# Optimization experiments

Measured on AMD Instinct MI355X. Metric: run time of the kernel, lower is better.

## Reference

```python
import jax, jax.numpy as jnp
import numpy as np
from jax import lax

RES = 14
DIM = 384
KEY_DIM = 32
NUM_HEADS = 12
ATTN_RATIO = 4
NH_KD = KEY_DIM * NUM_HEADS            # 384
DH = ATTN_RATIO * KEY_DIM * NUM_HEADS  # 1536
HQKV = DH + 2 * NH_KD                  # 2304
BN_EPS = 1e-5


def _bias_idxs():
    ys, xs = np.meshgrid(np.arange(RES), np.arange(RES), indexing='ij')
    ys = ys.reshape(-1); xs = xs.reshape(-1)
    dy = np.abs(ys[:, None] - ys[None, :])
    dx = np.abs(xs[:, None] - xs[None, :])
    return jnp.asarray(dy * RES + dx, dtype=jnp.int32)  # [196,196], 196 unique offsets


def setup_inputs() -> dict:
    key = jax.random.key(0)
    ks = jax.random.split(key, 16)
    B = 128
    x = jax.random.normal(ks[0], (B, DIM, RES, RES), dtype=jnp.float32)
    # qkv: 1x1 conv DIM->HQKV + BN
    qkv_w = jax.random.normal(ks[1], (HQKV, DIM, 1, 1), dtype=jnp.float32) * 0.05
    qkv_g = jax.random.normal(ks[2], (HQKV,), dtype=jnp.float32) * 0.1 + 1.0
    qkv_b = jax.random.normal(ks[3], (HQKV,), dtype=jnp.float32) * 0.1
    qkv_m = jax.random.normal(ks[4], (HQKV,), dtype=jnp.float32) * 0.1
    qkv_v = jax.random.uniform(ks[5], (HQKV,), dtype=jnp.float32) + 0.5
    # dw: depthwise 3x3 conv on q channels + BN
    dw_w = jax.random.normal(ks[6], (NH_KD, 1, 3, 3), dtype=jnp.float32) * 0.2
    dw_g = jax.random.normal(ks[7], (NH_KD,), dtype=jnp.float32) * 0.1 + 1.0
    dw_b = jax.random.normal(ks[8], (NH_KD,), dtype=jnp.float32) * 0.1
    dw_m = jax.random.normal(ks[9], (NH_KD,), dtype=jnp.float32) * 0.1
    dw_v = jax.random.uniform(ks[10], (NH_KD,), dtype=jnp.float32) + 0.5
    # proj: ReLU -> 1x1 conv DH->DIM + BN
    proj_w = jax.random.normal(ks[11], (DIM, DH, 1, 1), dtype=jnp.float32) * 0.05
    proj_g = jax.random.normal(ks[12], (DIM,), dtype=jnp.float32) * 0.1 + 1.0
    proj_b = jax.random.normal(ks[13], (DIM,), dtype=jnp.float32) * 0.1
    proj_m = jax.random.normal(ks[14], (DIM,), dtype=jnp.float32) * 0.1
    proj_v = jax.random.uniform(ks[15], (DIM,), dtype=jnp.float32) + 0.5
    ab = jax.random.normal(jax.random.fold_in(key, 99), (NUM_HEADS, RES * RES), dtype=jnp.float32) * 0.1
    return {
        'x': x,
        'qkv_w': qkv_w, 'qkv_g': qkv_g, 'qkv_b': qkv_b, 'qkv_m': qkv_m, 'qkv_v': qkv_v,
        'dw_w': dw_w, 'dw_g': dw_g, 'dw_b': dw_b, 'dw_m': dw_m, 'dw_v': dw_v,
        'proj_w': proj_w, 'proj_g': proj_g, 'proj_b': proj_b, 'proj_m': proj_m, 'proj_v': proj_v,
        'attn_biases': ab,
        'bias_idxs': _bias_idxs(),
    }


def _bn(x, g, b, m, v):
    scale = g / jnp.sqrt(v + BN_EPS)
    return x * scale[None, :, None, None] + (b - m * scale)[None, :, None, None]


def reference(x, qkv_w, qkv_g, qkv_b, qkv_m, qkv_v,
              dw_w, dw_g, dw_b, dw_m, dw_v,
              proj_w, proj_g, proj_b, proj_m, proj_v,
              attn_biases, bias_idxs):
    B, _, H, W = x.shape
    n = H * W
    scale = KEY_DIM ** -0.5
    # 1x1 conv + BN
    qkv = jnp.einsum('bchw,oc->bohw', x, qkv_w[:, :, 0, 0])
    qkv = _bn(qkv, qkv_g, qkv_b, qkv_m, qkv_v)
    q = qkv[:, :NH_KD]
    k = qkv[:, NH_KD:2 * NH_KD]
    v = qkv[:, 2 * NH_KD:]
    # depthwise 3x3 conv + BN on q
    q = lax.conv_general_dilated(q, dw_w, (1, 1), ((1, 1), (1, 1)),
                                 dimension_numbers=('NCHW', 'OIHW', 'NCHW'),
                                 feature_group_count=NH_KD)
    q = _bn(q, dw_g, dw_b, dw_m, dw_v)
    # heads: [b, h, d, n]
    q = q.reshape(B, NUM_HEADS, KEY_DIM, n)
    k = k.reshape(B, NUM_HEADS, KEY_DIM, n)
    v = v.reshape(B, NUM_HEADS, ATTN_RATIO * KEY_DIM, n)
    bias = attn_biases[:, bias_idxs]  # [h, n, n]
    attn = jnp.einsum('bhdn,bhdm->bhnm', q, k) * scale + bias[None]
    attn = jax.nn.softmax(attn, axis=-1)
    out = jnp.einsum('bhdm,bhnm->bhdn', v, attn).reshape(B, DH, H, W)
    out = jax.nn.relu(out)
    out = jnp.einsum('bchw,oc->bohw', out, proj_w[:, :, 0, 0])
    return _bn(out, proj_g, proj_b, proj_m, proj_v)
```

## Files before the change

kernel.cpp:

```cpp
#include <hip/hip_runtime.h>

typedef __bf16 bf16;
typedef bf16 bf16x8 __attribute__((ext_vector_type(8)));
typedef bf16 bf16x4 __attribute__((ext_vector_type(4)));
typedef short short4v __attribute__((ext_vector_type(4)));
typedef float f32x4 __attribute__((ext_vector_type(4)));

#define NPIX 196
#define CIN 384
#define NHEADS 12
#define MPAD 224
#define VSTRIDE 232
#define OSTRIDE 40

__device__ __forceinline__ float ldf(const void* p, size_t i, int f) {
    return f ? ((const float*)p)[i] : (float)((const bf16*)p)[i];
}

__device__ __forceinline__ void gld16(const void* g, void* lds_wave_base) {
    __builtin_amdgcn_global_load_lds(
        (const __attribute__((address_space(1))) void*)(unsigned long long)g,
        (__attribute__((address_space(3))) void*)(unsigned long long)lds_wave_base,
        16, 0, 0);
}

__device__ __forceinline__ int xcd_swizzle(int orig, int nwg) {
    int q = nwg >> 3, r = nwg & 7;
    int xcd = orig & 7, idx = orig >> 3;
    return (xcd < r ? xcd * (q + 1) : r * (q + 1) + (xcd - r) * q) + idx;
}

__device__ __forceinline__ f32x4 mfma16(bf16x4 a, bf16x4 b, f32x4 c) {
#if __has_builtin(__builtin_amdgcn_mfma_f32_16x16x16bf16_1k)
    return __builtin_amdgcn_mfma_f32_16x16x16bf16_1k(
        __builtin_bit_cast(short4v, a), __builtin_bit_cast(short4v, b), c, 0, 0, 0);
#else
    asm volatile("v_mfma_f32_16x16x16_bf16 %0, %1, %2, %0" : "+v"(c) : "v"(a), "v"(b));
    return c;
#endif
}

__device__ __forceinline__ f32x4 vmax4(f32x4 a, f32x4 b) {
    f32x4 r;
    r[0] = fmaxf(a[0], b[0]);
    r[1] = fmaxf(a[1], b[1]);
    r[2] = fmaxf(a[2], b[2]);
    r[3] = fmaxf(a[3], b[3]);
    return r;
}

__global__ void detect_kernel(const unsigned int* __restrict__ x, int* __restrict__ flag) {
    __shared__ int cnt;
    if (threadIdx.x == 0) cnt = 0;
    __syncthreads();
    int c = 0;
#pragma unroll
    for (int k = 0; k < 8; k++) {
        unsigned int w = x[threadIdx.x * 8 + k];
        unsigned int e = (w >> 7) & 0xFFu;
        if (e > 200u) c++;
    }
    atomicAdd(&cnt, c);
    __syncthreads();
    if (threadIdx.x == 0) *flag = (cnt >= 16) ? 1 : 0;
}

__global__ void convert_kernel(const void* __restrict__ src, bf16* __restrict__ dst, int n,
                               const int* __restrict__ flag) {
    int f = *flag;
    for (int i = blockIdx.x * 256 + threadIdx.x; i < n; i += gridDim.x * 256)
        dst[i] = (bf16)ldf(src, i, f);
}

__global__ void transpose_x_kernel(const void* __restrict__ x, const int* __restrict__ flag,
                                   bf16* __restrict__ xt, int b0) {
    __shared__ bf16 tile[32][33];
    int f = *flag;
    int b = blockIdx.z, gb = b0 + b;
    int c0 = blockIdx.y * 32;
    int hw0 = blockIdx.x * 32;
    int tx = threadIdx.x, ty = threadIdx.y;
    int hw = hw0 + tx, c = c0 + ty;
    if (hw < NPIX) tile[ty][tx] = (bf16)ldf(x, ((size_t)gb * CIN + c) * NPIX + hw, f);
    __syncthreads();
    int hw2 = hw0 + ty, c2 = c0 + tx;
    if (hw2 < NPIX) xt[((size_t)b * NPIX + hw2) * CIN + c2] = tile[tx][ty];
}

__device__ __forceinline__ void gemm_tile(const bf16* __restrict__ A, const bf16* __restrict__ B,
                                          int K, bf16* As, bf16* Bs, f32x4 acc[4][4]) {
    int tid = threadIdx.x;
    int wave = tid >> 6, lane = tid & 63;
    int wm = wave >> 1, wn = wave & 1;
    int row = lane & 15, grp = lane >> 4;
    int sr = lane >> 3;
    int scg = (lane & 7) ^ sr;
    const int BUF = 128 * 64;
    const bf16* Ag = A + (size_t)(wave * 8 + sr) * K + scg * 8;
    const bf16* Bg = B + (size_t)(wave * 8 + sr) * K + scg * 8;
#pragma unroll
    for (int p = 0; p < 4; p++) {
        gld16(Ag + (size_t)(p * 32) * K, As + (p * 256 + wave * 64) * 8);
        gld16(Bg + (size_t)(p * 32) * K, Bs + (p * 256 + wave * 64) * 8);
    }
    __syncthreads();
    int cur = 0;
    for (int kb = 0; kb < K; kb += 64) {
        if (kb + 64 < K) {
            bf16* Asn = As + (cur ^ 1) * BUF;
            bf16* Bsn = Bs + (cur ^ 1) * BUF;
#pragma unroll
            for (int p = 0; p < 4; p++) {
                gld16(Ag + (size_t)(p * 32) * K + kb + 64, Asn + (p * 256 + wave * 64) * 8);
                gld16(Bg + (size_t)(p * 32) * K + kb + 64, Bsn + (p * 256 + wave * 64) * 8);
            }
        }
        const bf16* Asc = As + cur * BUF;
        const bf16* Bsc = Bs + cur * BUF;
#pragma unroll
        for (int ki = 0; ki < 2; ki++) {
            bf16x8 af[4], bfr[4];
#pragma unroll
            for (int t = 0; t < 4; t++) {
                int ra = wm * 64 + t * 16 + row;
                af[t] = *(const bf16x8*)(Asc + ra * 64 + (((ki * 4 + grp) ^ (ra & 7)) * 8));
                int rb = wn * 64 + t * 16 + row;
                bfr[t] = *(const bf16x8*)(Bsc + rb * 64 + (((ki * 4 + grp) ^ (rb & 7)) * 8));
            }
#pragma unroll
            for (int mt = 0; mt < 4; mt++)
#pragma unroll
                for (int nt = 0; nt < 4; nt++)
                    acc[mt][nt] =
                        __builtin_amdgcn_mfma_f32_16x16x32_bf16(af[mt], bfr[nt], acc[mt][nt], 0, 0, 0);
        }
        if (kb + 64 < K) {
            __syncthreads();
            cur ^= 1;
        }
    }
}

__global__ __launch_bounds__(256) void gemm_qkv_kernel(
    const bf16* __restrict__ xt, const bf16* __restrict__ w,
    const void* __restrict__ g, const void* __restrict__ bb,
    const void* __restrict__ mm, const void* __restrict__ vv, const int* __restrict__ flag,
    bf16* __restrict__ qb, bf16* __restrict__ kt, bf16* __restrict__ vb) {
    __shared__ bf16 As[2 * 128 * 64];
    __shared__ bf16 Bs[2 * 128 * 64];
    f32x4 acc[4][4];
#pragma unroll
    for (int i = 0; i < 4; i++)
#pragma unroll
        for (int j = 0; j < 4; j++) acc[i][j] = (f32x4){0.f, 0.f, 0.f, 0.f};
    int nwg = gridDim.x * gridDim.y;
    int l = xcd_swizzle(blockIdx.y * gridDim.x + blockIdx.x, nwg);
    int m0 = (l % gridDim.x) * 128, n0 = (l / gridDim.x) * 128;
    gemm_tile(w + (size_t)m0 * CIN, xt + (size_t)n0 * CIN, CIN, As, Bs, acc);
    int f = *flag;
    int wave = threadIdx.x >> 6, lane = threadIdx.x & 63;
    int wm = wave >> 1, wn = wave & 1, row = lane & 15, grp = lane >> 4;
#pragma unroll
    for (int mt = 0; mt < 4; mt++) {
#pragma unroll
        for (int r = 0; r < 4; r++) {
            int o = m0 + wm * 64 + mt * 16 + grp * 4 + r;
            float scv = ldf(g, o, f) * rsqrtf(ldf(vv, o, f) + 1e-5f);
            float sh = ldf(bb, o, f) - ldf(mm, o, f) * scv;
#pragma unroll
            for (int nt = 0; nt < 4; nt++) {
                int n = n0 + wn * 64 + nt * 16 + row;
                int b = n / NPIX, hw = n - b * NPIX;
                float val = acc[mt][nt][r] * scv + sh;
                bf16 bv = (bf16)val;
                if (o < 384) {
                    qb[((size_t)b * 384 + o) * NPIX + hw] = bv;
                } else if (o < 768) {
                    kt[((size_t)b * NPIX + hw) * CIN + (o - 384)] = bv;
                } else {
                    vb[((size_t)b * 1536 + (o - 768)) * MPAD + hw] = bv;
                }
            }
        }
    }
}

__global__ __launch_bounds__(256) void gemm_proj_kernel(
    const bf16* __restrict__ ot, const bf16* __restrict__ w,
    const void* __restrict__ g, const void* __restrict__ bb,
    const void* __restrict__ mm, const void* __restrict__ vv, const int* __restrict__ flag,
    void* __restrict__ out, int b0) {
    __shared__ bf16 As[2 * 128 * 64];
    __shared__ bf16 Bs[2 * 128 * 64];
    f32x4 acc[4][4];
#pragma unroll
    for (int i = 0; i < 4; i++)
#pragma unroll
        for (int j = 0; j < 4; j++) acc[i][j] = (f32x4){0.f, 0.f, 0.f, 0.f};
    int nwg = gridDim.x * gridDim.y;
    int l = xcd_swizzle(blockIdx.y * gridDim.x + blockIdx.x, nwg);
    int m0 = (l % gridDim.x) * 128, n0 = (l / gridDim.x) * 128;
    gemm_tile(w + (size_t)m0 * 1536, ot + (size_t)n0 * 1536, 1536, As, Bs, acc);
    int f = *flag;
    int wave = threadIdx.x >> 6, lane = threadIdx.x & 63;
    int wm = wave >> 1, wn = wave & 1, row = lane & 15, grp = lane >> 4;
#pragma unroll
    for (int mt = 0; mt < 4; mt++) {
#pragma unroll
        for (int r = 0; r < 4; r++) {
            int o = m0 + wm * 64 + mt * 16 + grp * 4 + r;
            float scv = ldf(g, o, f) * rsqrtf(ldf(vv, o, f) + 1e-5f);
            float sh = ldf(bb, o, f) - ldf(mm, o, f) * scv;
#pragma unroll
            for (int nt = 0; nt < 4; nt++) {
                int n = n0 + wn * 64 + nt * 16 + row;
                int b = n / NPIX, hw = n - b * NPIX;
                float val = acc[mt][nt][r] * scv + sh;
                size_t oidx = ((size_t)(b0 + b) * 384 + o) * NPIX + hw;
                if (f) ((float*)out)[oidx] = val;
                else ((bf16*)out)[oidx] = (bf16)val;
            }
        }
    }
}

__global__ void dwconv_kernel(const bf16* __restrict__ qb, const bf16* __restrict__ w,
                              const void* __restrict__ g, const void* __restrict__ bb,
                              const void* __restrict__ mm, const void* __restrict__ vv,
                              const int* __restrict__ flag, bf16* __restrict__ qt) {
    __shared__ bf16 tile[32][33];
    int f = *flag;
    int b = blockIdx.z;
    int c0 = blockIdx.y * 32, hw0 = blockIdx.x * 32;
    int tx = threadIdx.x, ty = threadIdx.y;
    int c = c0 + ty, hw = hw0 + tx;
    if (hw < NPIX) {
        int y = hw / 14, x = hw % 14;
        float acc = 0.f;
        const bf16* wp = w + c * 9;
        const bf16* qp = qb + ((size_t)b * 384 + c) * NPIX;
#pragma unroll
        for (int ky = 0; ky < 3; ky++) {
            int yy = y + ky - 1;
            if (yy < 0 || yy >= 14) continue;
#pragma unroll
            for (int kx = 0; kx < 3; kx++) {
                int xx = x + kx - 1;
                if (xx < 0 || xx >= 14) continue;
                acc += (float)qp[yy * 14 + xx] * (float)wp[ky * 3 + kx];
            }
        }
        float sc = ldf(g, c, f) * rsqrtf(ldf(vv, c, f) + 1e-5f);
        float sh = ldf(bb, c, f) - ldf(mm, c, f) * sc;
        tile[ty][tx] = (bf16)(acc * sc + sh);
    }
    __syncthreads();
    int hw2 = hw0 + ty, c2 = c0 + tx;
    if (hw2 < NPIX) qt[((size_t)b * NPIX + hw2) * CIN + c2] = tile[tx][ty];
}

__global__ void bias_gather_kernel(const void* __restrict__ ab, const int* __restrict__ idx,
                                   const int* __restrict__ flag, float* __restrict__ biasf) {
    int f = *flag;
    int t = blockIdx.x * 256 + threadIdx.x;
    if (t >= NHEADS * NPIX * MPAD) return;
    int h = t / (NPIX * MPAD);
    int rem = t - h * (NPIX * MPAD);
    int n = rem / MPAD, m = rem - n * MPAD;
    biasf[t] = (m < NPIX) ? ldf(ab, h * NPIX + idx[n * NPIX + m], f) : -1e30f;
}

__global__ void zero_vpad_kernel(bf16* __restrict__ vb, int rows) {
    int t = blockIdx.x * 256 + threadIdx.x;
    if (t >= rows * 7) return;
    int r = t / 7, c = t - r * 7;
    *(unsigned long long*)(vb + (size_t)r * MPAD + NPIX + c * 4) = 0ull;
}

__global__ __launch_bounds__(256, 2) void attn_kernel(
    const bf16* __restrict__ qt, const bf16* __restrict__ ktp, const bf16* __restrict__ vb,
    const float* __restrict__ biasf, bf16* __restrict__ ot) {
    __shared__ bf16 Vs[128 * VSTRIDE];
    __shared__ bf16 Osh[4][16 * OSTRIDE];
    int nwg = gridDim.x * gridDim.y;
    int l = xcd_swizzle(blockIdx.y * gridDim.x + blockIdx.x, nwg);
    int h = l % NHEADS, b = l / NHEADS;
    int tid = threadIdx.x;
    int wave = tid >> 6, lane = tid & 63;
    int row = lane & 15, grp = lane >> 4;
    const float scale = 0.17677669529663687f;
    const f32x4 zf = {0.f, 0.f, 0.f, 0.f};

    {
        const bf16* vsrc = vb + ((size_t)b * 1536 + h * 128) * MPAD;
#pragma unroll
        for (int it = 0; it < 14; it++) {
            int i = it * 256 + tid;
            int r = i / 28, gch = i - r * 28;
            *(bf16x8*)(Vs + r * VSTRIDE + gch * 8) = *(const bf16x8*)(vsrc + (size_t)i * 8);
        }
    }
    __syncthreads();

    const bf16* vls = Vs + row * VSTRIDE + grp * 4;

    for (int nb = wave; nb < 13; nb += 4) {
        int n0 = nb * 16;
        int n = n0 + row;
        int nc = n > 195 ? 195 : n;

        bf16x8 aq = *(const bf16x8*)(qt + ((size_t)b * NPIX + nc) * CIN + h * 32 + grp * 8);

        f32x4 sacc[14];
#pragma unroll
        for (int mt = 0; mt < 14; mt++) {
            int krow = mt * 16 + row;
            if (krow > 195) krow = 195;
            bf16x8 ak = *(const bf16x8*)(ktp + ((size_t)b * NPIX + krow) * CIN + h * 32 + grp * 8);
            sacc[mt] = __builtin_amdgcn_mfma_f32_16x16x32_bf16(ak, aq, zf, 0, 0, 0);
        }

        const float* bp = biasf + ((size_t)h * NPIX + nc) * MPAD + grp * 4;
        f32x4 mxv = {-3.4e38f, -3.4e38f, -3.4e38f, -3.4e38f};
#pragma unroll
        for (int mt = 0; mt < 14; mt++) {
            f32x4 bv = *(const f32x4*)(bp + mt * 16);
            f32x4 s = sacc[mt] * scale + bv;
            sacc[mt] = s;
            mxv = vmax4(mxv, s);
        }
        float mx = fmaxf(fmaxf(mxv[0], mxv[1]), fmaxf(mxv[2], mxv[3]));
        mx = fmaxf(mx, __shfl_xor(mx, 16));
        mx = fmaxf(mx, __shfl_xor(mx, 32));

        f32x4 sumv = zf;
        bf16x4 pf[14];
#pragma unroll
        for (int mt = 0; mt < 14; mt++) {
            f32x4 e;
#pragma unroll
            for (int r = 0; r < 4; r++) e[r] = __expf(sacc[mt][r] - mx);
            sumv += e;
            bf16x4 pb;
#pragma unroll
            for (int r = 0; r < 4; r++) pb[r] = (bf16)e[r];
            pf[mt] = pb;
        }
        float sum = (sumv[0] + sumv[1]) + (sumv[2] + sumv[3]);
        sum += __shfl_xor(sum, 16);
        sum += __shfl_xor(sum, 32);
        float inv = 1.f / sum;

        f32x4 oacc[8];
#pragma unroll
        for (int dt = 0; dt < 8; dt++) oacc[dt] = zf;
#pragma unroll
        for (int mt = 0; mt < 14; mt++) {
            bf16x4 p = pf[mt];
#pragma unroll
            for (int dt = 0; dt < 8; dt++) {
                bf16x4 v4 = *(const bf16x4*)(vls + dt * 16 * VSTRIDE + mt * 16);
                oacc[dt] = mfma16(v4, p, oacc[dt]);
            }
        }

        bf16* osw = Osh[wave];
        int r2 = lane >> 2, c2 = lane & 3;
        int n2 = n0 + r2;
        bf16* op = ot + ((size_t)b * NPIX + n2) * 1536 + h * 128;
#pragma unroll
        for (int dp = 0; dp < 4; dp++) {
#pragma unroll
            for (int u = 0; u < 2; u++) {
                int dt = dp * 2 + u;
                bf16x4 o4;
#pragma unroll
                for (int r = 0; r < 4; r++) {
                    float v = oacc[dt][r] * inv;
                    o4[r] = (bf16)(v > 0.f ? v : 0.f);
                }
                *(bf16x4*)(osw + row * OSTRIDE + u * 16 + grp * 4) = o4;
            }
            asm volatile("s_waitcnt lgkmcnt(0)" ::: "memory");
            if (n2 < NPIX) {
                bf16x8 ov = *(const bf16x8*)(osw + r2 * OSTRIDE + c2 * 8);
                *(bf16x8*)(op + dp * 32 + c2 * 8) = ov;
            }
            asm volatile("s_waitcnt lgkmcnt(0)" ::: "memory");
        }
    }
}

extern "C" void kernel_launch(void* const* d_in, const int* in_sizes, int n_in,
                              void* d_out, int out_size, void* d_ws, size_t ws_size,
                              hipStream_t stream) {
    const void* x      = d_in[0];
    const void* qkv_w  = d_in[1];
    const void* qkv_g  = d_in[2];
    const void* qkv_b  = d_in[3];
    const void* qkv_m  = d_in[4];
    const void* qkv_v  = d_in[5];
    const void* dw_w   = d_in[6];
    const void* dw_g   = d_in[7];
    const void* dw_b   = d_in[8];
    const void* dw_m   = d_in[9];
    const void* dw_v   = d_in[10];
    const void* proj_w = d_in[11];
    const void* proj_g = d_in[12];
    const void* proj_b = d_in[13];
    const void* proj_m = d_in[14];
    const void* proj_v = d_in[15];
    const void* ab     = d_in[16];
    const int*  idx    = (const int*)d_in[17];

    char* ws = (char*)d_ws;
    size_t off = 0;
    auto alloc = [&](size_t bytes) { void* p = ws + off; off += (bytes + 255) & ~(size_t)255; return p; };

    int*   flag = (int*)alloc(4);
    bf16*  wq   = (bf16*)alloc((size_t)2304 * 384 * 2);
    bf16*  wp   = (bf16*)alloc((size_t)384 * 1536 * 2);
    bf16*  wd   = (bf16*)alloc((size_t)384 * 9 * 2);
    float* biasf= (float*)alloc((size_t)NHEADS * NPIX * MPAD * 4);
    size_t fixed = off;

    const size_t s_xt = (size_t)NPIX * CIN;
    const size_t s_qb = (size_t)384 * NPIX;
    const size_t s_kt = (size_t)NPIX * 384;
    const size_t s_vb = (size_t)1536 * MPAD;
    const size_t s_ot = (size_t)NPIX * 1536;
    const size_t per_image = (s_xt + s_qb + s_kt + s_vb + s_ot) * 2;

    int CB = 128;
    while (CB > 32 && fixed + (size_t)CB * per_image > ws_size) CB >>= 1;

    bf16* xt  = (bf16*)alloc((size_t)CB * s_xt * 2);
    bf16* qb  = (bf16*)alloc((size_t)CB * s_qb * 2);
    bf16* ktp = (bf16*)alloc((size_t)CB * s_kt * 2);
    bf16* vb  = (bf16*)alloc((size_t)CB * s_vb * 2);
    bf16* ot  = (bf16*)alloc((size_t)CB * s_ot * 2);
    bf16* qt  = xt;

    detect_kernel<<<dim3(1), dim3(256), 0, stream>>>((const unsigned int*)x, flag);
    convert_kernel<<<dim3(256), dim3(256), 0, stream>>>(qkv_w, wq, 2304 * 384, flag);
    convert_kernel<<<dim3(256), dim3(256), 0, stream>>>(proj_w, wp, 384 * 1536, flag);
    convert_kernel<<<dim3(4), dim3(256), 0, stream>>>(dw_w, wd, 384 * 9, flag);
    int bg = (NHEADS * NPIX * MPAD + 255) / 256;
    bias_gather_kernel<<<dim3(bg), dim3(256), 0, stream>>>(ab, idx, flag, biasf);
    int vrows = CB * 1536;
    zero_vpad_kernel<<<dim3((vrows * 7 + 255) / 256), dim3(256), 0, stream>>>(vb, vrows);

    dim3 tb(32, 32);
    for (int b0 = 0; b0 < 128; b0 += CB) {
        int cb = (128 - b0 < CB) ? (128 - b0) : CB;
        int ntiles = (cb * NPIX) / 128;
        transpose_x_kernel<<<dim3(7, 12, cb), tb, 0, stream>>>(x, flag, xt, b0);
        gemm_qkv_kernel<<<dim3(18, ntiles), dim3(256), 0, stream>>>(xt, wq, qkv_g, qkv_b, qkv_m,
                                                                    qkv_v, flag, qb, ktp, vb);
        dwconv_kernel<<<dim3(7, 12, cb), tb, 0, stream>>>(qb, wd, dw_g, dw_b, dw_m, dw_v, flag, qt);
        attn_kernel<<<dim3(NHEADS, cb), dim3(256), 0, stream>>>(qt, ktp, vb, biasf, ot);
        gemm_proj_kernel<<<dim3(3, ntiles), dim3(256), 0, stream>>>(ot, wp, proj_g, proj_b, proj_m,
                                                                    proj_v, flag, d_out, b0);
    }
}
```

Measured before the change: 488.0 us.

## Overlap GEMM prefetch with explicit vmcnt waits and stage K-transpose stores via LDS

The GEMM main loop replaces full __syncthreads with s_waitcnt vmcnt(8) plus s_barrier and sched barriers. This lets the next tile's global-to-LDS loads stay in flight while the current tile is computed. The A and B buffers are merged into one shared array so it can be reused. In the QKV GEMM, the K-projection tiles are written into LDS transposed and then stored to global memory as coalesced 16-byte rows, instead of strided 2-byte scatters. The exact vmcnt count relies on the global_load_lds issue count per thread, and an extra LDS round trip is added.

```diff
diff --git a/kernel.cpp b/kernel.cpp
--- a/kernel.cpp
+++ b/kernel.cpp
@@ -12,6 +12,7 @@
 #define MPAD 224
 #define VSTRIDE 232
 #define OSTRIDE 40
+#define TSTRIDE 136
 
 __device__ __forceinline__ float ldf(const void* p, size_t i, int f) {
     return f ? ((const float*)p)[i] : (float)((const bf16*)p)[i];
@@ -88,7 +89,7 @@
 }
 
 __device__ __forceinline__ void gemm_tile(const bf16* __restrict__ A, const bf16* __restrict__ B,
-                                          int K, bf16* As, bf16* Bs, f32x4 acc[4][4]) {
+                                          int K, bf16* smem, f32x4 acc[4][4]) {
     int tid = threadIdx.x;
     int wave = tid >> 6, lane = tid & 63;
     int wm = wave >> 1, wn = wave & 1;
@@ -96,6 +97,8 @@
     int sr = lane >> 3;
     int scg = (lane & 7) ^ sr;
     const int BUF = 128 * 64;
+    bf16* As = smem;
+    bf16* Bs = smem + 2 * BUF;
     const bf16* Ag = A + (size_t)(wave * 8 + sr) * K + scg * 8;
     const bf16* Bg = B + (size_t)(wave * 8 + sr) * K + scg * 8;
 #pragma unroll
@@ -103,8 +106,8 @@
         gld16(Ag + (size_t)(p * 32) * K, As + (p * 256 + wave * 64) * 8);
         gld16(Bg + (size_t)(p * 32) * K, Bs + (p * 256 + wave * 64) * 8);
     }
-    __syncthreads();
     int cur = 0;
+#pragma unroll 1
     for (int kb = 0; kb < K; kb += 64) {
         if (kb + 64 < K) {
             bf16* Asn = As + (cur ^ 1) * BUF;
@@ -114,7 +117,14 @@
                 gld16(Ag + (size_t)(p * 32) * K + kb + 64, Asn + (p * 256 + wave * 64) * 8);
                 gld16(Bg + (size_t)(p * 32) * K + kb + 64, Bsn + (p * 256 + wave * 64) * 8);
             }
-        }
+            __builtin_amdgcn_sched_barrier(0);
+            asm volatile("s_waitcnt vmcnt(8)" ::: "memory");
+        } else {
+            __builtin_amdgcn_sched_barrier(0);
+            asm volatile("s_waitcnt vmcnt(0)" ::: "memory");
+        }
+        __builtin_amdgcn_s_barrier();
+        __builtin_amdgcn_sched_barrier(0);
         const bf16* Asc = As + cur * BUF;
         const bf16* Bsc = Bs + cur * BUF;
 #pragma unroll
@@ -134,11 +144,11 @@
                     acc[mt][nt] =
                         __builtin_amdgcn_mfma_f32_16x16x32_bf16(af[mt], bfr[nt], acc[mt][nt], 0, 0, 0);
         }
-        if (kb + 64 < K) {
-            __syncthreads();
-            cur ^= 1;
-        }
-    }
+        __builtin_amdgcn_sched_barrier(0);
+        __builtin_amdgcn_s_barrier();
+        cur ^= 1;
+    }
+    __builtin_amdgcn_sched_barrier(0);
 }
 
 __global__ __launch_bounds__(256) void gemm_qkv_kernel(
@@ -146,8 +156,7 @@
     const void* __restrict__ g, const void* __restrict__ bb,
     const void* __restrict__ mm, const void* __restrict__ vv, const int* __restrict__ flag,
     bf16* __restrict__ qb, bf16* __restrict__ kt, bf16* __restrict__ vb) {
-    __shared__ bf16 As[2 * 128 * 64];
-    __shared__ bf16 Bs[2 * 128 * 64];
+    __shared__ bf16 smem[4 * 128 * 64];
     f32x4 acc[4][4];
 #pragma unroll
     for (int i = 0; i < 4; i++)
@@ -156,29 +165,55 @@
     int nwg = gridDim.x * gridDim.y;
     int l = xcd_swizzle(blockIdx.y * gridDim.x + blockIdx.x, nwg);
     int m0 = (l % gridDim.x) * 128, n0 = (l / gridDim.x) * 128;
-    gemm_tile(w + (size_t)m0 * CIN, xt + (size_t)n0 * CIN, CIN, As, Bs, acc);
-    int f = *flag;
-    int wave = threadIdx.x >> 6, lane = threadIdx.x & 63;
+    gemm_tile(w + (size_t)m0 * CIN, xt + (size_t)n0 * CIN, CIN, smem, acc);
+    int f = *flag;
+    int tid = threadIdx.x;
+    int wave = tid >> 6, lane = tid & 63;
     int wm = wave >> 1, wn = wave & 1, row = lane & 15, grp = lane >> 4;
-#pragma unroll
-    for (int mt = 0; mt < 4; mt++) {
-#pragma unroll
-        for (int r = 0; r < 4; r++) {
-            int o = m0 + wm * 64 + mt * 16 + grp * 4 + r;
-            float scv = ldf(g, o, f) * rsqrtf(ldf(vv, o, f) + 1e-5f);
-            float sh = ldf(bb, o, f) - ldf(mm, o, f) * scv;
-#pragma unroll
-            for (int nt = 0; nt < 4; nt++) {
-                int n = n0 + wn * 64 + nt * 16 + row;
-                int b = n / NPIX, hw = n - b * NPIX;
-                float val = acc[mt][nt][r] * scv + sh;
-                bf16 bv = (bf16)val;
-                if (o < 384) {
-                    qb[((size_t)b * 384 + o) * NPIX + hw] = bv;
-                } else if (o < 768) {
-                    kt[((size_t)b * NPIX + hw) * CIN + (o - 384)] = bv;
-                } else {
-                    vb[((size_t)b * 1536 + (o - 768)) * MPAD + hw] = bv;
+    if (m0 >= 384 && m0 < 768) {
+        bf16* tbuf = smem;
+#pragma unroll
+        for (int mt = 0; mt < 4; mt++) {
+#pragma unroll
+            for (int r = 0; r < 4; r++) {
+                int ol = wm * 64 + mt * 16 + grp * 4 + r;
+                int o = m0 + ol;
+                float scv = ldf(g, o, f) * rsqrtf(ldf(vv, o, f) + 1e-5f);
+                float sh = ldf(bb, o, f) - ldf(mm, o, f) * scv;
+#pragma unroll
+                for (int nt = 0; nt < 4; nt++) {
+                    int nl = wn * 64 + nt * 16 + row;
+                    tbuf[nl * TSTRIDE + ol] = (bf16)(acc[mt][nt][r] * scv + sh);
+                }
+            }
+        }
+        __syncthreads();
+#pragma unroll
+        for (int it = 0; it < 8; it++) {
+            int g2 = it * 256 + tid;
+            int nl = g2 >> 4, ch = g2 & 15;
+            *(bf16x8*)(kt + (size_t)(n0 + nl) * CIN + (m0 - 384) + ch * 8) =
+                *(const bf16x8*)(tbuf + nl * TSTRIDE + ch * 8);
+        }
+    } else {
+#pragma unroll
+        for (int mt = 0; mt < 4; mt++) {
+#pragma unroll
+            for (int r = 0; r < 4; r++) {
+                int o = m0 + wm * 64 + mt * 16 + grp * 4 + r;
+                float scv = ldf(g, o, f) * rsqrtf(ldf(vv, o, f) + 1e-5f);
+                float sh = ldf(bb, o, f) - ldf(mm, o, f) * scv;
+#pragma unroll
+                for (int nt = 0; nt < 4; nt++) {
+                    int n = n0 + wn * 64 + nt * 16 + row;
+                    int b = n / NPIX, hw = n - b * NPIX;
+                    float val = acc[mt][nt][r] * scv + sh;
+                    bf16 bv = (bf16)val;
+                    if (o < 384) {
+                        qb[((size_t)b * 384 + o) * NPIX + hw] = bv;
+                    } else {
+                        vb[((size_t)b * 1536 + (o - 768)) * MPAD + hw] = bv;
+                    }
                 }
             }
         }
@@ -190,8 +225,7 @@
     const void* __restrict__ g, const void* __restrict__ bb,
     const void* __restrict__ mm, const void* __restrict__ vv, const int* __restrict__ flag,
     void* __restrict__ out, int b0) {
-    __shared__ bf16 As[2 * 128 * 64];
-    __shared__ bf16 Bs[2 * 128 * 64];
+    __shared__ bf16 smem[4 * 128 * 64];
     f32x4 acc[4][4];
 #pragma unroll
     for (int i = 0; i < 4; i++)
@@ -200,7 +234,7 @@
     int nwg = gridDim.x * gridDim.y;
     int l = xcd_swizzle(blockIdx.y * gridDim.x + blockIdx.x, nwg);
     int m0 = (l % gridDim.x) * 128, n0 = (l / gridDim.x) * 128;
-    gemm_tile(w + (size_t)m0 * 1536, ot + (size_t)n0 * 1536, 1536, As, Bs, acc);
+    gemm_tile(w + (size_t)m0 * 1536, ot + (size_t)n0 * 1536, 1536, smem, acc);
     int f = *flag;
     int wave = threadIdx.x >> 6, lane = threadIdx.x & 63;
     int wm = wave >> 1, wn = wave & 1, row = lane & 15, grp = lane >> 4;
```

Result: faster. 446.9 us (-8.4%).
